# Kernel optimization log

Hardware: AMD Instinct MI355X
Metric: run time of the kernel (lower is better)

The kernel has to match this reference:

```python
import jax, jax.numpy as jnp
import numpy as np

HIDDEN = 1024
HEADS = 16
HEAD = HIDDEN // HEADS
EXPAND = 4096
EPS = 1e-5


def layer_norm(x, g, b):
    mu = jnp.mean(x, axis=-1, keepdims=True)
    var = jnp.mean((x - mu) ** 2, axis=-1, keepdims=True)
    return (x - mu) * jax.lax.rsqrt(var + EPS) * g + b


def setup_inputs() -> dict:
    key = jax.random.key(0)
    ks = jax.random.split(key, 12)
    s = 0.02
    return {
        "x": jax.random.normal(ks[0], (4, 2048, HIDDEN), dtype=jnp.float32),
        "Wqkv": jax.random.normal(ks[1], (HIDDEN, 3 * HIDDEN), dtype=jnp.float32) * s,
        "bqkv": jnp.zeros((3 * HIDDEN,), jnp.float32),
        "Wproj": jax.random.normal(ks[2], (HIDDEN, HIDDEN), dtype=jnp.float32) * s,
        "bproj": jnp.zeros((HIDDEN,), jnp.float32),
        "W1": jax.random.normal(ks[3], (HIDDEN, EXPAND), dtype=jnp.float32) * s,
        "b1": jnp.zeros((EXPAND,), jnp.float32),
        "W2": jax.random.normal(ks[4], (EXPAND, HIDDEN), dtype=jnp.float32) * s,
        "b2": jnp.zeros((HIDDEN,), jnp.float32),
        "g1": jnp.ones((HIDDEN,), jnp.float32),
        "be1": jnp.zeros((HIDDEN,), jnp.float32),
        "g2": jnp.ones((HIDDEN,), jnp.float32),
        "be2": jnp.zeros((HIDDEN,), jnp.float32),
    }


def attention(x, Wqkv, bqkv, Wproj, bproj):
    B, L, _ = x.shape
    qkv = (x @ Wqkv + bqkv).reshape(B, L, 3, HEADS, HEAD)
    q, k, v = [qkv[:, :, i].transpose(0, 2, 1, 3) for i in range(3)]  # [B,H,L,D]
    attn = jnp.einsum("bnld,bnkd->bnlk", q, k) / np.sqrt(HEAD).astype(np.float32)
    attn = jax.nn.softmax(attn, axis=-1)
    o = jnp.einsum("bnlk,bnkd->bnld", attn, v)
    o = o.transpose(0, 2, 1, 3).reshape(B, L, HIDDEN)
    return o @ Wproj + bproj


def reference(x, Wqkv, bqkv, Wproj, bproj, W1, b1, W2, b2, g1, be1, g2, be2):
    # post-norm transformer block (pre_norm=False), dropout=0 (eval)
    h = layer_norm(x + attention(x, Wqkv, bqkv, Wproj, bproj), g1, be1)
    ff = jax.nn.gelu(h @ W1 + b1, approximate=False) @ W2 + b2
    return layer_norm(h + ff, g2, be2)
```

## Files before the change

### kernel.cpp

```cpp
#include <hip/hip_runtime.h>
#include <hip/hip_bf16.h>
#include <math.h>


typedef __bf16 bf16_t;
typedef __bf16 bf16x8 __attribute__((ext_vector_type(8)));
typedef __bf16 bf16x4 __attribute__((ext_vector_type(4)));
typedef float f32x4 __attribute__((ext_vector_type(4)));
typedef float f32x16 __attribute__((ext_vector_type(16)));

#define HID   1024
#define NHEAD 16
#define HD    64
#define EXPD  4096
#define LSEQ  2048
#define BATCH 4
#define MROWS (BATCH * LSEQ)

#if __has_builtin(__builtin_amdgcn_exp2f)
#define EXP2F __builtin_amdgcn_exp2f
#else
#define EXP2F exp2f
#endif

__device__ __forceinline__ void gld_lds16(const bf16_t* g, bf16_t* l) {
  __builtin_amdgcn_global_load_lds(
      (const __attribute__((address_space(1))) void*)g,
      (__attribute__((address_space(3))) void*)l, 16, 0, 0);
}

__device__ __forceinline__ void vmwait(int n) {
  if (n == 8)      asm volatile("s_waitcnt vmcnt(8)" ::: "memory");
  else if (n == 4) asm volatile("s_waitcnt vmcnt(4)" ::: "memory");
  else if (n == 3) asm volatile("s_waitcnt vmcnt(3)" ::: "memory");
  else if (n == 0) asm volatile("s_waitcnt vmcnt(0)" ::: "memory");
}

__device__ __forceinline__ void block_bar() {
  asm volatile("" ::: "memory");
  __builtin_amdgcn_s_barrier();
  asm volatile("" ::: "memory");
}

__device__ __forceinline__ void swap32(unsigned& a, unsigned& b) {
#if __has_builtin(__builtin_amdgcn_permlane32_swap)
  auto r = __builtin_amdgcn_permlane32_swap(a, b, false, false);
  a = r[0]; b = r[1];
#else
  bool hiL = ((threadIdx.x & 63) >= 32);
  unsigned pa = (unsigned)__shfl_xor((int)a, 32, 64);
  unsigned pb = (unsigned)__shfl_xor((int)b, 32, 64);
  unsigned na = hiL ? pb : a;
  unsigned nb = hiL ? b : pa;
  a = na; b = nb;
#endif
}

__device__ __forceinline__ unsigned pk_bf16(float lo, float hi) {
  bf16_t l = (bf16_t)lo, h = (bf16_t)hi;
  unsigned short ul, uh;
  __builtin_memcpy(&ul, &l, 2);
  __builtin_memcpy(&uh, &h, 2);
  return (unsigned)ul | ((unsigned)uh << 16);
}

__global__ __launch_bounds__(256) void cvt_bf16(const float* __restrict__ in,
                                                bf16_t* __restrict__ out, int n4) {
  int i = blockIdx.x * 256 + threadIdx.x;
  if (i >= n4) return;
  float4 v = ((const float4*)in)[i];
  bf16x4 o;
  o[0] = (bf16_t)v.x; o[1] = (bf16_t)v.y; o[2] = (bf16_t)v.z; o[3] = (bf16_t)v.w;
  ((bf16x4*)out)[i] = o;
}

__global__ __launch_bounds__(256) void transpose_cvt(const float* __restrict__ W,
                                                     bf16_t* __restrict__ Wt,
                                                     int K, int N) {
  __shared__ float tile[32][33];
  int n0 = blockIdx.x * 32, k0 = blockIdx.y * 32;
  int tx = threadIdx.x & 31, ty = threadIdx.x >> 5;
#pragma unroll
  for (int i = 0; i < 32; i += 8)
    tile[ty + i][tx] = W[(size_t)(k0 + ty + i) * N + n0 + tx];
  __syncthreads();
#pragma unroll
  for (int i = 0; i < 32; i += 8)
    Wt[(size_t)(n0 + ty + i) * K + k0 + tx] = (bf16_t)tile[tx][ty + i];
}

__global__ __launch_bounds__(256) void transpose_v(const bf16_t* __restrict__ qkvb,
                                                   bf16_t* __restrict__ vT) {
  __shared__ bf16_t tile[64][65];
  const int l0 = blockIdx.x * 64;
  const int bh = blockIdx.y;
  const int b = bh >> 4, h = bh & 15;
  const int tx = threadIdx.x & 63, ty = threadIdx.x >> 6;
  const bf16_t* src = qkvb + ((size_t)(b * LSEQ + l0)) * 3072 + 2048 + h * 64;
#pragma unroll
  for (int i = 0; i < 16; ++i) {
    int l = ty + 4 * i;
    tile[l][tx] = src[(size_t)l * 3072 + tx];
  }
  __syncthreads();
  bf16_t* dst = vT + ((size_t)bh * HD) * LSEQ + l0;
#pragma unroll
  for (int i = 0; i < 16; ++i) {
    int d = ty + 4 * i;
    dst[(size_t)d * LSEQ + tx] = tile[tx][d];
  }
}

template <int BM, int BN, int NTHR>
__global__ __launch_bounds__(NTHR, (NTHR == 512 ? 4 : 3))
void gemm_k(const bf16_t* __restrict__ A,
            const bf16_t* __restrict__ Bt,
            const float* __restrict__ bias,
            void* __restrict__ C,
            float* __restrict__ C2,
            int M, int N, int K, int mode) {
  constexpr int WC = (NTHR / 64) / 2;
  constexpr int AL = BM * 4 / NTHR;
  constexpr int BL = BN * 4 / NTHR;
  constexpr int LOADS = AL + BL;
  constexpr int RSTEP = NTHR >> 2;
  __shared__ bf16_t As[3 * BM * 32];
  __shared__ bf16_t Bs[3 * BN * 32];

  const int nbx = gridDim.x;
  int p = blockIdx.y * nbx + blockIdx.x;
  const int GM = 8;
  int group = p / (GM * nbx);
  int idx = p - group * (GM * nbx);
  const int by = group * GM + (idx & (GM - 1));
  const int bx = idx >> 3;
  const int n0 = bx * BN, m0 = by * BM;

  const int zz = blockIdx.z;
  const int kLen = K / (int)gridDim.z;
  const int kOff = zz * kLen;

  const int t = threadIdx.x;
  const int lane = t & 63, w = t >> 6;
  const int wr = w / WC, wc = w % WC;
  const int quad = lane >> 4, l16 = lane & 15;

  f32x4 acc[4][4];
#pragma unroll
  for (int i = 0; i < 4; ++i)
#pragma unroll
    for (int j = 0; j < 4; ++j) acc[i][j] = (f32x4){0.f, 0.f, 0.f, 0.f};

  const int r0 = t >> 2;
  const unsigned ksw = (((unsigned)t & 3u) ^ ((unsigned)(r0 >> 1) & 3u)) * 8u;
  const unsigned offR0 = (unsigned)r0 * (unsigned)K + ksw;

  const bf16_t* aB = A + (size_t)m0 * K + kOff;
  const bf16_t* bB = Bt + (size_t)n0 * K + kOff;

  unsigned aoff[4], boff[4];
#pragma unroll
  for (int i = 0; i < 4; ++i) {
    int row = wr * 64 + 16 * i + l16;
    aoff[i] = (unsigned)(row * 32 + (quad ^ ((row >> 1) & 3)) * 8);
  }
#pragma unroll
  for (int j = 0; j < 4; ++j) {
    int row = wc * 64 + 16 * j + l16;
    boff[j] = (unsigned)(row * 32 + (quad ^ ((row >> 1) & 3)) * 8);
  }

  auto stage = [&](int slot, int kk) {
    bf16_t* Asl = As + slot * (BM * 32);
    bf16_t* Bsl = Bs + slot * (BN * 32);
    const bf16_t* aS = aB + kk;
    const bf16_t* bS = bB + kk;
#pragma unroll
    for (int a = 0; a < AL; ++a)
      gld_lds16(aS + offR0 + (size_t)a * RSTEP * K, Asl + (t + a * NTHR) * 8);
#pragma unroll
    for (int b = 0; b < BL; ++b)
      gld_lds16(bS + offR0 + (size_t)b * RSTEP * K, Bsl + (t + b * NTHR) * 8);
  };

  const int NT = kLen >> 5;

  stage(0, 0);
  stage(1, 32);
  vmwait(LOADS);
  block_bar();

  int cs = 0;
  for (int kt = 0; kt < NT; ++kt) {
    if (kt < NT - 2) {
      int ss = cs == 0 ? 2 : cs - 1;
      stage(ss, (kt + 2) * 32);
    }
    const bf16_t* Asl = As + cs * (BM * 32);
    const bf16_t* Bsl = Bs + cs * (BN * 32);
    bf16x8 af[4], bfr[4];
#pragma unroll
    for (int i = 0; i < 4; ++i) af[i] = *(const bf16x8*)(Asl + aoff[i]);
#pragma unroll
    for (int j = 0; j < 4; ++j) bfr[j] = *(const bf16x8*)(Bsl + boff[j]);
    __builtin_amdgcn_s_setprio(1);
#pragma unroll
    for (int i = 0; i < 4; ++i)
#pragma unroll
      for (int j = 0; j < 4; ++j)
        acc[i][j] = __builtin_amdgcn_mfma_f32_16x16x32_bf16(af[i], bfr[j], acc[i][j], 0, 0, 0);
    __builtin_amdgcn_s_setprio(0);
    if (kt < NT - 2)      vmwait(LOADS);
    else if (kt == NT - 2) vmwait(0);
    if (kt < NT - 1) block_bar();
    cs = cs == 2 ? 0 : cs + 1;
  }

#pragma unroll
  for (int i = 0; i < 4; ++i) {
    int rowb = m0 + wr * 64 + 16 * i + quad * 4;
#pragma unroll
    for (int j = 0; j < 4; ++j) {
      int col = n0 + wc * 64 + 16 * j + l16;
      float bv = (zz == 0) ? bias[col] : 0.f;
#pragma unroll
      for (int r = 0; r < 4; ++r) {
        float v = acc[i][j][r] + bv;
        size_t idx = (size_t)(rowb + r) * N + col;
        if (zz != 0) {
          C2[idx] = v;
        } else if (mode == 0) {
          ((bf16_t*)C)[idx] = (bf16_t)v;
        } else if (mode == 1) {
          float u = v * (0.7978845608028654f + 0.0356774081f * v * v);
          float e = EXP2F(u * 2.885390082f);
          float th = (e - 1.f) / (e + 1.f);
          float gel = 0.5f * v * (1.f + th);
          ((bf16_t*)C)[idx] = (bf16_t)gel;
        } else {
          ((float*)C)[idx] = v;
        }
      }
    }
  }
}

__global__ __launch_bounds__(256, 2) void attn_kernel(const bf16_t* __restrict__ qkv,
                                                      const bf16_t* __restrict__ vT,
                                                      bf16_t* __restrict__ ob) {
  __shared__ bf16_t smem[5 * 128 * 64];
  bf16_t* Qs = smem + 32768;
  const int qt = blockIdx.x, h = blockIdx.y, b = blockIdx.z;
  const int t = threadIdx.x, lane = t & 63, w = t >> 6;
  const int l32 = lane & 31, hi = lane >> 5;
  const size_t RS = 3 * HID;
  const int bh = b * NHEAD + h;

  const bf16_t* qbase = qkv + ((size_t)(b * LSEQ + qt * 128)) * RS + h * HD;
  const bf16_t* kbase = qkv + ((size_t)b * LSEQ) * RS + HID + h * HD;
  const bf16_t* vtbase = vT + (size_t)bh * HD * LSEQ;

#pragma unroll
  for (int s = 0; s < 4; ++s) {
    int l = t + s * 256;
    int r = l >> 3, c8 = l & 7;
    gld_lds16(qbase + (size_t)r * RS + ((c8 ^ (r & 7)) * 8), Qs + l * 8);
  }
  __syncthreads();

  const float sc = 0.18033688011112042f;
  bf16x8 bq[4];
  {
    int qrow = 32 * w + l32;
#pragma unroll
    for (int c = 0; c < 4; ++c) {
      int y = 2 * c + hi;
      bf16x8 q8 = *(const bf16x8*)(Qs + qrow * 64 + ((y ^ (qrow & 7)) * 8));
#pragma unroll
      for (int e = 0; e < 8; ++e) q8[e] = (bf16_t)((float)q8[e] * sc);
      bq[c] = q8;
    }
  }

  auto stageKV = [&](int slot, int kt) {
    bf16_t* Ks = smem + slot * 16384;
    bf16_t* Vts = Ks + 8192;
#pragma unroll
    for (int s = 0; s < 4; ++s) {
      int l = t + s * 256;
      int r = l >> 3, c8 = l & 7;
      gld_lds16(kbase + (size_t)(kt * 128 + r) * RS + ((c8 ^ (r & 7)) * 8), Ks + l * 8);
      int rv = l >> 4, c16 = l & 15;
      gld_lds16(vtbase + (size_t)rv * LSEQ + kt * 128 + ((c16 ^ (rv & 7)) * 8), Vts + l * 8);
    }
  };

  f32x16 accO[2];
#pragma unroll
  for (int dt = 0; dt < 2; ++dt)
#pragma unroll
    for (int e = 0; e < 16; ++e) accO[dt][e] = 0.f;
  float l_acc = 0.f;

  constexpr int NT = LSEQ / 128;
  stageKV(0, 0);

  for (int kt = 0; kt < NT; ++kt) {
    const int cs = kt & 1;
    if (kt + 1 < NT) {
      stageKV(1 - cs, kt + 1);
      vmwait(8);
    } else {
      vmwait(0);
    }
    block_bar();
    const bf16_t* Ks = smem + cs * 16384;
    const bf16_t* Vts = Ks + 8192;

#pragma unroll
    for (int kt2 = 0; kt2 < 2; ++kt2) {
      f32x16 s0, s1;
#pragma unroll
      for (int e = 0; e < 16; ++e) { s0[e] = 0.f; s1[e] = 0.f; }
      __builtin_amdgcn_s_setprio(1);
#pragma unroll
      for (int c = 0; c < 4; ++c) {
        int y = 2 * c + hi;
        int r0 = (2 * kt2 + 0) * 32 + l32;
        bf16x8 a0 = *(const bf16x8*)(Ks + r0 * 64 + ((y ^ (r0 & 7)) * 8));
        s0 = __builtin_amdgcn_mfma_f32_32x32x16_bf16(a0, bq[c], s0, 0, 0, 0);
        int r1 = (2 * kt2 + 1) * 32 + l32;
        bf16x8 a1 = *(const bf16x8*)(Ks + r1 * 64 + ((y ^ (r1 & 7)) * 8));
        s1 = __builtin_amdgcn_mfma_f32_32x32x16_bf16(a1, bq[c], s1, 0, 0, 0);
      }
      __builtin_amdgcn_s_setprio(0);

      unsigned pf[2][2][4];
#pragma unroll
      for (int tile = 0; tile < 2; ++tile) {
        f32x16& sv = tile ? s1 : s0;
        float p[16];
#pragma unroll
        for (int e = 0; e < 16; ++e) { p[e] = EXP2F(sv[e]); l_acc += p[e]; }
        unsigned lo[4], hi_[4];
#pragma unroll
        for (int g = 0; g < 4; ++g) {
          lo[g] = pk_bf16(p[4 * g + 0], p[4 * g + 1]);
          hi_[g] = pk_bf16(p[4 * g + 2], p[4 * g + 3]);
        }
#pragma unroll
        for (int c2 = 0; c2 < 2; ++c2) {
          unsigned aL = lo[2 * c2], bL = lo[2 * c2 + 1];
          swap32(aL, bL);
          pf[tile][c2][0] = aL; pf[tile][c2][2] = bL;
          unsigned aH = hi_[2 * c2], bH = hi_[2 * c2 + 1];
          swap32(aH, bH);
          pf[tile][c2][1] = aH; pf[tile][c2][3] = bH;
        }
      }

      __builtin_amdgcn_s_setprio(1);
#pragma unroll
      for (int dt = 0; dt < 2; ++dt)
#pragma unroll
        for (int tile = 0; tile < 2; ++tile)
#pragma unroll
          for (int c2 = 0; c2 < 2; ++c2) {
            int ktile = 2 * kt2 + tile;
            int c8v = ktile * 4 + c2 * 2 + hi;
            int rv = dt * 32 + l32;
            bf16x8 av = *(const bf16x8*)(Vts + rv * 128 + ((c8v ^ (rv & 7)) * 8));
            union { unsigned u[4]; bf16x8 v; } bp;
            bp.u[0] = pf[tile][c2][0]; bp.u[1] = pf[tile][c2][1];
            bp.u[2] = pf[tile][c2][2]; bp.u[3] = pf[tile][c2][3];
            accO[dt] = __builtin_amdgcn_mfma_f32_32x32x16_bf16(av, bp.v, accO[dt], 0, 0, 0);
          }
      __builtin_amdgcn_s_setprio(0);
    }
    block_bar();
  }

  l_acc += __shfl_xor(l_acc, 32, 64);
  float inv = 1.f / l_acc;

  bf16_t* Osh = smem;
  {
    int q = 32 * w + l32;
#pragma unroll
    for (int dt = 0; dt < 2; ++dt)
#pragma unroll
      for (int e = 0; e < 16; ++e) {
        int d = dt * 32 + (e & 3) + 8 * (e >> 2) + 4 * hi;
        Osh[q * 68 + d] = (bf16_t)(accO[dt][e] * inv);
      }
  }
  __syncthreads();
#pragma unroll
  for (int s = 0; s < 4; ++s) {
    int l = t + s * 256;
    int r = l >> 3, c8 = l & 7;
    bf16x8 v = *(const bf16x8*)(Osh + r * 68 + c8 * 8);
    *(bf16x8*)(ob + ((size_t)(b * LSEQ + qt * 128 + r)) * HID + h * HD + c8 * 8) = v;
  }
}

__global__ __launch_bounds__(256) void resid_ln(const float* __restrict__ X,
                                                const float* __restrict__ Y,
                                                const float* __restrict__ Y2,
                                                const float* __restrict__ g,
                                                const float* __restrict__ be,
                                                float* __restrict__ outf,
                                                bf16_t* __restrict__ outb) {
  const int row = blockIdx.x;
  const int t = threadIdx.x;
  float4 a = ((const float4*)X)[(size_t)row * 256 + t];
  float4 bvec = ((const float4*)Y)[(size_t)row * 256 + t];
  float4 cvec = {0.f, 0.f, 0.f, 0.f};
  if (Y2) cvec = ((const float4*)Y2)[(size_t)row * 256 + t];
  float v0 = a.x + bvec.x + cvec.x, v1 = a.y + bvec.y + cvec.y;
  float v2 = a.z + bvec.z + cvec.z, v3 = a.w + bvec.w + cvec.w;
  float s = v0 + v1 + v2 + v3;
  float s2 = v0 * v0 + v1 * v1 + v2 * v2 + v3 * v3;
#pragma unroll
  for (int msk = 1; msk < 64; msk <<= 1) {
    s += __shfl_xor(s, msk, 64);
    s2 += __shfl_xor(s2, msk, 64);
  }
  __shared__ float red[8];
  int w = t >> 6;
  if ((t & 63) == 0) { red[w] = s; red[w + 4] = s2; }
  __syncthreads();
  s = red[0] + red[1] + red[2] + red[3];
  s2 = red[4] + red[5] + red[6] + red[7];
  float mu = s * (1.f / 1024.f);
  float var = s2 * (1.f / 1024.f) - mu * mu;
  float rstd = rsqrtf(var + 1e-5f);
  float4 gg = ((const float4*)g)[t];
  float4 bb = ((const float4*)be)[t];
  float o0 = (v0 - mu) * rstd * gg.x + bb.x;
  float o1 = (v1 - mu) * rstd * gg.y + bb.y;
  float o2 = (v2 - mu) * rstd * gg.z + bb.z;
  float o3 = (v3 - mu) * rstd * gg.w + bb.w;
  float4 o = {o0, o1, o2, o3};
  ((float4*)outf)[(size_t)row * 256 + t] = o;
  if (outb) {
    bf16x4 ob4;
    ob4[0] = (bf16_t)o0; ob4[1] = (bf16_t)o1; ob4[2] = (bf16_t)o2; ob4[3] = (bf16_t)o3;
    ((bf16x4*)outb)[(size_t)row * 256 + t] = ob4;
  }
}

extern "C" void kernel_launch(void* const* d_in, const int* in_sizes, int n_in,
                              void* d_out, int out_size, void* d_ws, size_t ws_size,
                              hipStream_t stream) {
  const float* x     = (const float*)d_in[0];
  const float* Wqkv  = (const float*)d_in[1];
  const float* bqkv  = (const float*)d_in[2];
  const float* Wproj = (const float*)d_in[3];
  const float* bproj = (const float*)d_in[4];
  const float* W1    = (const float*)d_in[5];
  const float* b1    = (const float*)d_in[6];
  const float* W2    = (const float*)d_in[7];
  const float* b2    = (const float*)d_in[8];
  const float* g1    = (const float*)d_in[9];
  const float* be1   = (const float*)d_in[10];
  const float* g2    = (const float*)d_in[11];
  const float* be2   = (const float*)d_in[12];
  float* out = (float*)d_out;

  char* ws = (char*)d_ws;
  bf16_t* w2T    = (bf16_t*)(ws);
  float*  h      = (float*) (ws + ((size_t)8 << 20));
  float*  a_f2   = (float*) (ws + ((size_t)40 << 20));
  bf16_t* qkv_ff = (bf16_t*)(ws + ((size_t)72 << 20));
  char*   E      = ws + ((size_t)136 << 20);
  bf16_t* wqkvT  = (bf16_t*)(E);
  bf16_t* wprojT = (bf16_t*)(E + ((size_t)6 << 20));
  bf16_t* w1T    = (bf16_t*)(E + ((size_t)8 << 20));
  char*   xb_ob  = E + ((size_t)16 << 20);
  bf16_t* hb     = (bf16_t*)(E + ((size_t)32 << 20));
  float*  f2b    = (float*)E;

  bf16_t* xb    = (bf16_t*)xb_ob;
  bf16_t* ob    = (bf16_t*)xb_ob;
  bf16_t* qkvb  = qkv_ff;
  bf16_t* ff1b  = qkv_ff;
  float*  attnf = a_f2;
  float*  ff2f  = a_f2;
  bf16_t* vTg   = hb;

  dim3 blk(256);
  dim3 blk512(512);
  transpose_cvt<<<dim3(3072 / 32, 1024 / 32), blk, 0, stream>>>(Wqkv, wqkvT, 1024, 3072);
  transpose_cvt<<<dim3(1024 / 32, 1024 / 32), blk, 0, stream>>>(Wproj, wprojT, 1024, 1024);
  transpose_cvt<<<dim3(4096 / 32, 1024 / 32), blk, 0, stream>>>(W1, w1T, 1024, 4096);
  transpose_cvt<<<dim3(1024 / 32, 4096 / 32), blk, 0, stream>>>(W2, w2T, 4096, 1024);
  cvt_bf16<<<MROWS * HID / 4 / 256, blk, 0, stream>>>(x, xb, MROWS * HID / 4);

  gemm_k<128, 256, 512><<<dim3(3072 / 256, MROWS / 128), blk512, 0, stream>>>(
      xb, wqkvT, bqkv, qkvb, nullptr, MROWS, 3072, 1024, 0);
  transpose_v<<<dim3(LSEQ / 64, BATCH * NHEAD), blk, 0, stream>>>(qkvb, vTg);
  attn_kernel<<<dim3(LSEQ / 128, NHEAD, BATCH), blk, 0, stream>>>(qkvb, vTg, ob);
  gemm_k<128, 128, 256><<<dim3(1024 / 128, MROWS / 128), blk, 0, stream>>>(
      ob, wprojT, bproj, attnf, nullptr, MROWS, 1024, 1024, 2);
  resid_ln<<<MROWS, blk, 0, stream>>>(x, attnf, nullptr, g1, be1, h, hb);
  gemm_k<128, 256, 512><<<dim3(4096 / 256, MROWS / 128), blk512, 0, stream>>>(
      hb, w1T, b1, ff1b, nullptr, MROWS, 4096, 1024, 1);
  gemm_k<128, 256, 512><<<dim3(1024 / 256, MROWS / 128, 2), blk512, 0, stream>>>(
      ff1b, w2T, b2, ff2f, f2b, MROWS, 1024, 4096, 2);
  resid_ln<<<MROWS, blk, 0, stream>>>(h, ff2f, f2b, g2, be2, out, (bf16_t*)nullptr);
}
```

Measured before the change: 550.5 us.

## Fuse V transpose into QKV GEMM, split-K proj GEMM, add 256x256 FF1 GEMM

The QKV GEMM epilogue now writes the V columns directly in transposed per-head layout, so the separate transpose_v kernel is removed. The output-projection GEMM switches to a split-K grid of 2, writing partials into the h buffer, which resid_ln then sums. A new 256x256-tile GEMM with 512 threads, double-buffered two-half K stages and a GELU epilogue replaces the generic kernel for the FF1 matmul, aiming for more operand reuse per block. Reusing h as a split-K scratch buffer while resid_ln also writes h in place carries an aliasing risk.

```diff
diff --git a/kernel.cpp b/kernel.cpp
--- a/kernel.cpp
+++ b/kernel.cpp
@@ -64,6 +64,13 @@
   return (unsigned)ul | ((unsigned)uh << 16);
 }
 
+__device__ __forceinline__ float gelu_t(float v) {
+  float u = v * (0.7978845608028654f + 0.0356774081f * v * v);
+  float e = EXP2F(u * 2.885390082f);
+  float th = (e - 1.f) / (e + 1.f);
+  return 0.5f * v * (1.f + th);
+}
+
 __global__ __launch_bounds__(256) void cvt_bf16(const float* __restrict__ in,
                                                 bf16_t* __restrict__ out, int n4) {
   int i = blockIdx.x * 256 + threadIdx.x;
@@ -89,28 +96,6 @@
     Wt[(size_t)(n0 + ty + i) * K + k0 + tx] = (bf16_t)tile[tx][ty + i];
 }
 
-__global__ __launch_bounds__(256) void transpose_v(const bf16_t* __restrict__ qkvb,
-                                                   bf16_t* __restrict__ vT) {
-  __shared__ bf16_t tile[64][65];
-  const int l0 = blockIdx.x * 64;
-  const int bh = blockIdx.y;
-  const int b = bh >> 4, h = bh & 15;
-  const int tx = threadIdx.x & 63, ty = threadIdx.x >> 6;
-  const bf16_t* src = qkvb + ((size_t)(b * LSEQ + l0)) * 3072 + 2048 + h * 64;
-#pragma unroll
-  for (int i = 0; i < 16; ++i) {
-    int l = ty + 4 * i;
-    tile[l][tx] = src[(size_t)l * 3072 + tx];
-  }
-  __syncthreads();
-  bf16_t* dst = vT + ((size_t)bh * HD) * LSEQ + l0;
-#pragma unroll
-  for (int i = 0; i < 16; ++i) {
-    int d = ty + 4 * i;
-    dst[(size_t)d * LSEQ + tx] = tile[tx][d];
-  }
-}
-
 template <int BM, int BN, int NTHR>
 __global__ __launch_bounds__(NTHR, (NTHR == 512 ? 4 : 3))
 void gemm_k(const bf16_t* __restrict__ A,
@@ -118,6 +103,7 @@
             const float* __restrict__ bias,
             void* __restrict__ C,
             float* __restrict__ C2,
+            bf16_t* __restrict__ vTo,
             int M, int N, int K, int mode) {
   constexpr int WC = (NTHR / 64) / 2;
   constexpr int AL = BM * 4 / NTHR;
@@ -216,6 +202,9 @@
     cs = cs == 2 ? 0 : cs + 1;
   }
 
+  const bool vpath = (vTo != nullptr) && (n0 >= 2048);
+  const int bb = m0 >> 11;
+  const int l0b = m0 & 2047;
 #pragma unroll
   for (int i = 0; i < 4; ++i) {
     int rowb = m0 + wr * 64 + 16 * i + quad * 4;
@@ -223,6 +212,15 @@
     for (int j = 0; j < 4; ++j) {
       int col = n0 + wc * 64 + 16 * j + l16;
       float bv = (zz == 0) ? bias[col] : 0.f;
+      if (vpath) {
+        int hh = (col - 2048) >> 6, dd = (col - 2048) & 63;
+        int l0 = (rowb - m0) + l0b;
+        bf16x4 pk;
+#pragma unroll
+        for (int r = 0; r < 4; ++r) pk[r] = (bf16_t)(acc[i][j][r] + bv);
+        *(bf16x4*)(vTo + ((size_t)((bb * 16 + hh) * 64 + dd)) * 2048 + l0) = pk;
+        continue;
+      }
 #pragma unroll
       for (int r = 0; r < 4; ++r) {
         float v = acc[i][j][r] + bv;
@@ -232,14 +230,145 @@
         } else if (mode == 0) {
           ((bf16_t*)C)[idx] = (bf16_t)v;
         } else if (mode == 1) {
-          float u = v * (0.7978845608028654f + 0.0356774081f * v * v);
-          float e = EXP2F(u * 2.885390082f);
-          float th = (e - 1.f) / (e + 1.f);
-          float gel = 0.5f * v * (1.f + th);
-          ((bf16_t*)C)[idx] = (bf16_t)gel;
+          ((bf16_t*)C)[idx] = (bf16_t)gelu_t(v);
         } else {
           ((float*)C)[idx] = v;
         }
+      }
+    }
+  }
+}
+
+__global__ __launch_bounds__(512, 2)
+void gemm_8x(const bf16_t* __restrict__ A,
+             const bf16_t* __restrict__ Bt,
+             const float* __restrict__ bias,
+             bf16_t* __restrict__ C,
+             int M, int N, int K) {
+  __shared__ bf16_t smem[65536];
+  const int nbx = gridDim.x;
+  int p = blockIdx.y * nbx + blockIdx.x;
+  const int GM = 8;
+  int group = p / (GM * nbx);
+  int idx = p - group * (GM * nbx);
+  const int by = group * GM + (idx & (GM - 1));
+  const int bx = idx >> 3;
+  const int n0 = bx * 256, m0 = by * 256;
+
+  const int t = threadIdx.x;
+  const int lane = t & 63, w = t >> 6;
+  const int wr = w >> 2, wc = w & 3;
+  const int quad = lane >> 4, l16 = lane & 15;
+
+  f32x4 acc[8][4];
+#pragma unroll
+  for (int i = 0; i < 8; ++i)
+#pragma unroll
+    for (int j = 0; j < 4; ++j) acc[i][j] = (f32x4){0.f, 0.f, 0.f, 0.f};
+
+  const int r0 = t >> 2;
+  const unsigned ksw = (((unsigned)t & 3u) ^ ((unsigned)(r0 >> 1) & 3u)) * 8u;
+  const unsigned offR = (unsigned)r0 * (unsigned)K + ksw;
+
+  const bf16_t* aB = A + (size_t)m0 * K;
+  const bf16_t* bB = Bt + (size_t)n0 * K;
+
+  unsigned aoff[8], boff[4];
+#pragma unroll
+  for (int i = 0; i < 8; ++i) {
+    int row = wr * 128 + 16 * i + l16;
+    aoff[i] = (unsigned)(row * 32 + (quad ^ ((row >> 1) & 3)) * 8);
+  }
+#pragma unroll
+  for (int j = 0; j < 4; ++j) {
+    int row = wc * 64 + 16 * j + l16;
+    boff[j] = (unsigned)(16384 + row * 32 + (quad ^ ((row >> 1) & 3)) * 8);
+  }
+
+  auto stageChunk = [&](const bf16_t* src, int kk, int regionElem) {
+    bf16_t* d = smem + regionElem;
+    gld_lds16(src + kk + offR, d + t * 8);
+    gld_lds16(src + kk + offR + (size_t)128 * K, d + t * 8 + 4096);
+  };
+
+  const int NT = K >> 6;
+
+  stageChunk(aB, 0, 0);
+  stageChunk(bB, 0, 16384);
+  stageChunk(aB, 32, 8192);
+  stageChunk(bB, 32, 24576);
+  vmwait(4);
+  block_bar();
+
+  for (int kt = 0; kt < NT; ++kt) {
+    const int sb = (kt & 1) * 32768;
+    const int ss = ((kt + 1) & 1) * 32768;
+    const int ktk = (kt + 1) * 64;
+    const bool st = (kt + 1 < NT);
+    bf16x8 af[8], b0, b1;
+#pragma unroll
+    for (int i = 0; i < 8; ++i) af[i] = *(const bf16x8*)(smem + sb + aoff[i]);
+    b0 = *(const bf16x8*)(smem + sb + boff[0]);
+    b1 = *(const bf16x8*)(smem + sb + boff[1]);
+    if (st) stageChunk(aB, ktk, ss);
+    __builtin_amdgcn_s_setprio(1);
+#pragma unroll
+    for (int i = 0; i < 8; ++i) {
+      acc[i][0] = __builtin_amdgcn_mfma_f32_16x16x32_bf16(af[i], b0, acc[i][0], 0, 0, 0);
+      acc[i][1] = __builtin_amdgcn_mfma_f32_16x16x32_bf16(af[i], b1, acc[i][1], 0, 0, 0);
+    }
+    __builtin_amdgcn_s_setprio(0);
+    b0 = *(const bf16x8*)(smem + sb + boff[2]);
+    b1 = *(const bf16x8*)(smem + sb + boff[3]);
+    if (st) stageChunk(bB, ktk, ss + 16384);
+    __builtin_amdgcn_s_setprio(1);
+#pragma unroll
+    for (int i = 0; i < 8; ++i) {
+      acc[i][2] = __builtin_amdgcn_mfma_f32_16x16x32_bf16(af[i], b0, acc[i][2], 0, 0, 0);
+      acc[i][3] = __builtin_amdgcn_mfma_f32_16x16x32_bf16(af[i], b1, acc[i][3], 0, 0, 0);
+    }
+    __builtin_amdgcn_s_setprio(0);
+    if (st) vmwait(4); else vmwait(0);
+    block_bar();
+#pragma unroll
+    for (int i = 0; i < 8; ++i) af[i] = *(const bf16x8*)(smem + sb + 8192 + aoff[i]);
+    b0 = *(const bf16x8*)(smem + sb + 8192 + boff[0]);
+    b1 = *(const bf16x8*)(smem + sb + 8192 + boff[1]);
+    if (st) stageChunk(aB, ktk + 32, ss + 8192);
+    __builtin_amdgcn_s_setprio(1);
+#pragma unroll
+    for (int i = 0; i < 8; ++i) {
+      acc[i][0] = __builtin_amdgcn_mfma_f32_16x16x32_bf16(af[i], b0, acc[i][0], 0, 0, 0);
+      acc[i][1] = __builtin_amdgcn_mfma_f32_16x16x32_bf16(af[i], b1, acc[i][1], 0, 0, 0);
+    }
+    __builtin_amdgcn_s_setprio(0);
+    b0 = *(const bf16x8*)(smem + sb + 8192 + boff[2]);
+    b1 = *(const bf16x8*)(smem + sb + 8192 + boff[3]);
+    if (st) stageChunk(bB, ktk + 32, ss + 24576);
+    __builtin_amdgcn_s_setprio(1);
+#pragma unroll
+    for (int i = 0; i < 8; ++i) {
+      acc[i][2] = __builtin_amdgcn_mfma_f32_16x16x32_bf16(af[i], b0, acc[i][2], 0, 0, 0);
+      acc[i][3] = __builtin_amdgcn_mfma_f32_16x16x32_bf16(af[i], b1, acc[i][3], 0, 0, 0);
+    }
+    __builtin_amdgcn_s_setprio(0);
+    if (st) {
+      vmwait(4);
+      block_bar();
+    }
+  }
+
+#pragma unroll
+  for (int i = 0; i < 8; ++i) {
+    int rowb = m0 + wr * 128 + 16 * i + quad * 4;
+#pragma unroll
+    for (int j = 0; j < 4; ++j) {
+      int col = n0 + wc * 64 + 16 * j + l16;
+      float bv = bias[col];
+#pragma unroll
+      for (int r = 0; r < 4; ++r) {
+        float v = acc[i][j][r] + bv;
+        C[(size_t)(rowb + r) * N + col] = (bf16_t)gelu_t(v);
       }
     }
   }
@@ -498,15 +627,14 @@
   cvt_bf16<<<MROWS * HID / 4 / 256, blk, 0, stream>>>(x, xb, MROWS * HID / 4);
 
   gemm_k<128, 256, 512><<<dim3(3072 / 256, MROWS / 128), blk512, 0, stream>>>(
-      xb, wqkvT, bqkv, qkvb, nullptr, MROWS, 3072, 1024, 0);
-  transpose_v<<<dim3(LSEQ / 64, BATCH * NHEAD), blk, 0, stream>>>(qkvb, vTg);
+      xb, wqkvT, bqkv, qkvb, nullptr, vTg, MROWS, 3072, 1024, 0);
   attn_kernel<<<dim3(LSEQ / 128, NHEAD, BATCH), blk, 0, stream>>>(qkvb, vTg, ob);
-  gemm_k<128, 128, 256><<<dim3(1024 / 128, MROWS / 128), blk, 0, stream>>>(
-      ob, wprojT, bproj, attnf, nullptr, MROWS, 1024, 1024, 2);
-  resid_ln<<<MROWS, blk, 0, stream>>>(x, attnf, nullptr, g1, be1, h, hb);
-  gemm_k<128, 256, 512><<<dim3(4096 / 256, MROWS / 128), blk512, 0, stream>>>(
-      hb, w1T, b1, ff1b, nullptr, MROWS, 4096, 1024, 1);
+  gemm_k<128, 128, 256><<<dim3(1024 / 128, MROWS / 128, 2), blk, 0, stream>>>(
+      ob, wprojT, bproj, attnf, h, nullptr, MROWS, 1024, 1024, 2);
+  resid_ln<<<MROWS, blk, 0, stream>>>(x, attnf, h, g1, be1, h, hb);
+  gemm_8x<<<dim3(4096 / 256, MROWS / 256), blk512, 0, stream>>>(
+      hb, w1T, b1, ff1b, MROWS, 4096, 1024);
   gemm_k<128, 256, 512><<<dim3(1024 / 256, MROWS / 128, 2), blk512, 0, stream>>>(
-      ff1b, w2T, b2, ff2f, f2b, MROWS, 1024, 4096, 2);
+      ff1b, w2T, b2, ff2f, f2b, nullptr, MROWS, 1024, 4096, 2);
   resid_ln<<<MROWS, blk, 0, stream>>>(h, ff2f, f2b, g2, be2, out, (bf16_t*)nullptr);
 }
```

Result: slower. 573.0 us (+4.1%).
